# Kernel tuning notes

Hardware: AMD Instinct MI355X
Metric: run time of the kernel (lower is better)

## Reference

```python
import jax, jax.numpy as jnp
import numpy as np


def setup_inputs() -> dict:
    key = jax.random.key(0)
    k1, k2 = jax.random.split(key)
    qs = jax.random.normal(k1, (8, 4096, 1024), dtype=jnp.float32)      # [B, L, D]
    memory = jax.random.normal(k2, (512, 1024), dtype=jnp.float32)       # [M, D]
    return {"qs": qs, "memory": memory}


def reference(qs, memory):
    # s = qs @ memory.T  -> [B, L, M]; permute -> [B, M, L]
    s = jnp.einsum("bld,md->bml", qs, memory)
    # softmax over L (last dim after permute)
    v = jax.nn.softmax(s, axis=2)                 # [B, M, L]
    # r = v @ qs -> [B, M, D]
    r = jnp.einsum("bml,bld->bmd", v, qs)
    return (r, memory)
```

## Files before the change

kernel.cpp:

```cpp
#include <hip/hip_runtime.h>
#include <hip/hip_fp16.h>


#define B_ 8
#define L_ 4096
#define D_ 1024
#define M_ 512

typedef _Float16 halfT;
typedef _Float16 half8 __attribute__((ext_vector_type(8)));
typedef _Float16 half4_t __attribute__((ext_vector_type(4)));
typedef float f32x4 __attribute__((ext_vector_type(4)));

#define OFF_MEM16 0ull
#define SZ_MEM16  (512ull*1024*2)
#define OFF_QS16  (OFF_MEM16 + SZ_MEM16)
#define SZ_QS16   (8ull*4096*1024*2)
#define OFF_S     (OFF_QS16 + SZ_QS16)
#define SZ_S      (8ull*512*4096*4)
#define OFF_P16   (OFF_S + SZ_S)
#define SZ_P16    (8ull*512*4096*2)
#define OFF_INVL  (OFF_P16 + SZ_P16)
#define SZ_INVL   (8ull*512*4)
#define WS_NEED   (OFF_INVL + SZ_INVL)
#define OFF_RP    OFF_S

#define SWZ(n) ((((n)&7) ^ (((n)>>5)&7)))

__device__ __forceinline__ void gload_lds16(const halfT* g, halfT* l) {
  __builtin_amdgcn_global_load_lds(
      (const __attribute__((address_space(1))) unsigned int*)(const void*)g,
      (__attribute__((address_space(3))) unsigned int*)l, 16, 0, 0);
}

__global__ __launch_bounds__(256)
void prep_all(const float* __restrict__ qs, const float* __restrict__ mem,
              halfT* __restrict__ q16, halfT* __restrict__ mem16) {
  int bid = blockIdx.x;
  int tid = threadIdx.x;
  if (bid < 2048) {
    size_t base = (size_t)bid*256 + tid;
    #pragma unroll
    for (int it = 0; it < 8; ++it) {
      size_t i8 = base + (size_t)it*524288;
      size_t row = i8 >> 7;
      int c = (int)(i8 & 127);
      int kt = c >> 3, g = c & 7;
      const float* src = qs + i8*8;
      f32x4 x0 = *(const f32x4*)&src[0];
      f32x4 x1 = *(const f32x4*)&src[4];
      half8 h;
      #pragma unroll
      for (int j = 0; j < 4; ++j) { h[j] = (halfT)x0[j]; h[4+j] = (halfT)x1[j]; }
      *(half8*)&q16[row*1024 + kt*64 + ((g ^ ((int)row & 7)) << 3)] = h;
    }
  } else {
    int i8 = (bid - 2048)*256 + tid;
    int row = i8 >> 7, c = i8 & 127;
    int kt = c >> 3, g = c & 7;
    const float* src = mem + (size_t)i8*8;
    f32x4 x0 = *(const f32x4*)src;
    f32x4 x1 = *(const f32x4*)(src + 4);
    half8 h;
    #pragma unroll
    for (int j = 0; j < 4; ++j) { h[j] = (halfT)x0[j]; h[4+j] = (halfT)x1[j]; }
    *(half8*)&mem16[(size_t)row*1024 + kt*64 + ((g ^ (row & 7)) << 3)] = h;
  }
}

__global__ __launch_bounds__(512, 2)
void gemm_qk(const halfT* __restrict__ mem16, const halfT* __restrict__ qs16,
             float* __restrict__ S)
{
  __shared__ __attribute__((aligned(16))) halfT At[2][256*64];
  __shared__ __attribute__((aligned(16))) halfT Bt[2][256*64];

  int bid = blockIdx.x;
  int swz = (bid & 7)*32 + (bid >> 3);
  int b   = swz >> 5;
  int rem = swz & 31;
  int nt  = rem >> 1;
  int mt  = rem & 1;

  int tid = threadIdx.x;
  int w = tid >> 6, lane = tid & 63, lg = lane >> 4, li = lane & 15;
  int wm = w >> 2, wn = w & 3;
  int sl = li & 7;
  int rA = tid >> 3;
  int cA = (tid & 7)*8;

  const halfT* Ab = mem16 + (size_t)mt*256*1024;
  const halfT* Bb = qs16 + ((size_t)b*L_ + nt*256)*D_;

  f32x4 acc[8][4];
  #pragma unroll
  for (int i=0;i<8;++i)
    #pragma unroll
    for (int j=0;j<4;++j) acc[i][j] = (f32x4){0.f,0.f,0.f,0.f};

#define STAGE_QK(nb_, kt_)                                                     \
  do {                                                                         \
    const halfT* a0 = Ab + (size_t)(kt_)*64 + cA;                              \
    const halfT* b0 = Bb + (size_t)(kt_)*64 + cA;                              \
    _Pragma("unroll")                                                          \
    for (int j = 0; j < 4; ++j) {                                              \
      int r = rA + j*64;                                                       \
      gload_lds16(a0 + (size_t)r*1024, &At[nb_][(tid + j*512)*8]);             \
      gload_lds16(b0 + (size_t)r*1024, &Bt[nb_][(tid + j*512)*8]);             \
    }                                                                          \
  } while (0)

#define COMPUTE_QK(nb_)                                                        \
  do {                                                                         \
    _Pragma("unroll")                                                          \
    for (int ksub = 0; ksub < 2; ++ksub) {                                     \
      int gx = ((ksub*4 + lg) ^ sl) << 3;                                      \
      half8 Af[8], Bf[4];                                                      \
      _Pragma("unroll")                                                        \
      for (int mf = 0; mf < 8; ++mf)                                           \
        Af[mf] = *(const half8*)&At[nb_][(wm*128 + mf*16 + li)*64 + gx];       \
      _Pragma("unroll")                                                        \
      for (int nf = 0; nf < 4; ++nf)                                           \
        Bf[nf] = *(const half8*)&Bt[nb_][(wn*64 + nf*16 + li)*64 + gx];        \
      _Pragma("unroll")                                                        \
      for (int mf = 0; mf < 8; ++mf)                                           \
        _Pragma("unroll")                                                      \
        for (int nf = 0; nf < 4; ++nf)                                         \
          acc[mf][nf] = __builtin_amdgcn_mfma_f32_16x16x32_f16(Af[mf], Bf[nf], acc[mf][nf], 0,0,0); \
    }                                                                          \
  } while (0)

  STAGE_QK(0, 0);
  STAGE_QK(1, 1);
  asm volatile("s_waitcnt vmcnt(8)" ::: "memory");
  __builtin_amdgcn_sched_barrier(0);
  __builtin_amdgcn_s_barrier();

  for (int kt = 0; kt < 16; ++kt) {
    COMPUTE_QK(kt & 1);
    __builtin_amdgcn_s_barrier();
    if (kt + 2 < 16) {
      STAGE_QK(kt & 1, kt + 2);
      asm volatile("s_waitcnt vmcnt(8) lgkmcnt(0)" ::: "memory");
    } else {
      asm volatile("s_waitcnt vmcnt(0) lgkmcnt(0)" ::: "memory");
    }
    __builtin_amdgcn_sched_barrier(0);
    __builtin_amdgcn_s_barrier();
  }
#undef STAGE_QK
#undef COMPUTE_QK

  float* Cb = S + (size_t)b*M_*L_;
  int colbase = nt*256 + wn*64;
  #pragma unroll
  for (int mf = 0; mf < 8; ++mf) {
    #pragma unroll
    for (int r = 0; r < 4; ++r) {
      int row = mt*256 + wm*128 + mf*16 + lg*4 + r;
      #pragma unroll
      for (int nf = 0; nf < 4; ++nf)
        Cb[(size_t)row*L_ + colbase + nf*16 + li] = acc[mf][nf][r];
    }
  }
}

__global__ __launch_bounds__(512, 2)
void gemm_pv(const halfT* __restrict__ P16, const halfT* __restrict__ qs16,
             halfT* __restrict__ rp16)
{
  __shared__ __attribute__((aligned(16))) halfT At[2][256*64];
  __shared__ __attribute__((aligned(16))) halfT Bt[2][256*64];

  int bid = blockIdx.x;
  int swz = (bid & 7)*32 + (bid >> 3);
  int ks  = swz >> 6;
  int rem = swz & 63;
  int b   = rem >> 3;
  int nt  = (rem >> 1) & 3;
  int mt  = rem & 1;

  int tid = threadIdx.x;
  int w = tid >> 6, lane = tid & 63, lg = lane >> 4, li = lane & 15;
  int wm = w >> 2, wn = w & 3;
  int sl = li & 7;

  const halfT* Ab = P16 + (size_t)b*M_*L_ + (size_t)mt*256*L_ + ks*1024;
  const halfT* Bb = qs16 + ((size_t)b*L_ + ks*1024)*D_ + nt*256;
  int krow = tid >> 3;
  int seg  = tid & 7;
  int rs   = krow & 7;

  f32x4 acc[8][4];
  #pragma unroll
  for (int i=0;i<8;++i)
    #pragma unroll
    for (int j=0;j<4;++j) acc[i][j] = (f32x4){0.f,0.f,0.f,0.f};

  half8 hx[4];

#define GLOADB_PV(kt_)                                                         \
  do {                                                                         \
    const halfT* rowp = Bb + (size_t)((kt_)*64 + krow)*D_ + (seg >> 1)*64;     \
    _Pragma("unroll")                                                          \
    for (int j = 0; j < 4; ++j)                                                \
      hx[j] = *(const half8*)(rowp + ((((seg & 1)*4 + j) ^ rs) << 3));         \
  } while (0)

#define STAGEA_PV(nb_, kt_)                                                    \
  do {                                                                         \
    const halfT* a0 = Ab + (size_t)(kt_)*64 + (tid & 7)*8;                     \
    _Pragma("unroll")                                                          \
    for (int j = 0; j < 4; ++j)                                                \
      gload_lds16(a0 + (size_t)((tid >> 3) + j*64)*L_, &At[nb_][(tid + j*512)*8]); \
  } while (0)

#define WRITEB_PV(nb_)                                                         \
  do {                                                                         \
    _Pragma("unroll")                                                          \
    for (int i = 0; i < 32; ++i) {                                             \
      int n_ = seg*32 + i;                                                     \
      Bt[nb_][n_*64 + ((((krow >> 3) ^ SWZ(n_)) << 3)) + (krow & 7)] =         \
          hx[i >> 3][i & 7];                                                   \
    }                                                                          \
  } while (0)

#define COMPUTE_PV(nb_)                                                        \
  do {                                                                         \
    _Pragma("unroll")                                                          \
    for (int ksub = 0; ksub < 2; ++ksub) {                                     \
      int gx = ((ksub*4 + lg) ^ sl) << 3;                                      \
      half8 Af[8], Bf[4];                                                      \
      _Pragma("unroll")                                                        \
      for (int mf = 0; mf < 8; ++mf)                                           \
        Af[mf] = *(const half8*)&At[nb_][(wm*128 + mf*16 + li)*64 + gx];       \
      _Pragma("unroll")                                                        \
      for (int nf = 0; nf < 4; ++nf) {                                         \
        int n_ = wn*64 + nf*16 + li;                                           \
        Bf[nf] = *(const half8*)&Bt[nb_][n_*64 + (((ksub*4 + lg) ^ SWZ(n_)) << 3)]; \
      }                                                                        \
      _Pragma("unroll")                                                        \
      for (int mf = 0; mf < 8; ++mf)                                           \
        _Pragma("unroll")                                                      \
        for (int nf = 0; nf < 4; ++nf)                                         \
          acc[mf][nf] = __builtin_amdgcn_mfma_f32_16x16x32_f16(Af[mf], Bf[nf], acc[mf][nf], 0,0,0); \
    }                                                                          \
  } while (0)

  GLOADB_PV(0);
  STAGEA_PV(0, 0);
  STAGEA_PV(1, 1);
  WRITEB_PV(0);
  GLOADB_PV(1);
  asm volatile("s_waitcnt vmcnt(8) lgkmcnt(0)" ::: "memory");
  __builtin_amdgcn_sched_barrier(0);
  __builtin_amdgcn_s_barrier();

  for (int kt = 0; kt < 16; ++kt) {
    COMPUTE_PV(kt & 1);
    __builtin_amdgcn_s_barrier();
    if (kt + 1 < 16) WRITEB_PV((kt + 1) & 1);
    if (kt + 2 < 16) {
      GLOADB_PV(kt + 2);
      STAGEA_PV(kt & 1, kt + 2);
      asm volatile("s_waitcnt vmcnt(8) lgkmcnt(0)" ::: "memory");
    } else {
      asm volatile("s_waitcnt vmcnt(0) lgkmcnt(0)" ::: "memory");
    }
    __builtin_amdgcn_sched_barrier(0);
    __builtin_amdgcn_s_barrier();
  }
#undef GLOADB_PV
#undef STAGEA_PV
#undef WRITEB_PV
#undef COMPUTE_PV

  halfT* Cb = rp16 + (size_t)ks*((size_t)B_*M_*D_) + (size_t)b*M_*D_;
  int cpbase = nt*256 + wn*64 + li*4;
  #pragma unroll
  for (int mf = 0; mf < 8; ++mf) {
    #pragma unroll
    for (int r = 0; r < 4; ++r) {
      int row = mt*256 + wm*128 + mf*16 + lg*4 + r;
      half4_t hv;
      #pragma unroll
      for (int nf = 0; nf < 4; ++nf) hv[nf] = (halfT)acc[mf][nf][r];
      *(half4_t*)&Cb[(size_t)row*D_ + cpbase] = hv;
    }
  }
}

__global__ __launch_bounds__(256)
void softmax_rows(const float* __restrict__ S, halfT* __restrict__ P,
                  float* __restrict__ invl)
{
  int tid = threadIdx.x;
  int w = tid >> 6, lane = tid & 63;
  int row = blockIdx.x*4 + w;
  int rs  = row & 7;
  const float* src = S + (size_t)row*L_;
  f32x4 v[16];
  float mx = -3.0e38f;
  #pragma unroll
  for (int i = 0; i < 16; ++i) {
    v[i] = *(const f32x4*)&src[(size_t)(i*64 + lane)*4];
    #pragma unroll
    for (int e = 0; e < 4; ++e) mx = fmaxf(mx, v[i][e]);
  }
  #pragma unroll
  for (int off = 1; off < 64; off <<= 1) mx = fmaxf(mx, __shfl_xor(mx, off));

  float sum = 0.f;
  halfT* dst = P + (size_t)row*L_;
  #pragma unroll
  for (int i = 0; i < 16; ++i) {
    half4_t h;
    #pragma unroll
    for (int e = 0; e < 4; ++e) {
      float ev = __expf(v[i][e] - mx);
      sum += ev;
      h[e] = (halfT)ev;
    }
    int c = i*64 + lane;
    int kt = c >> 4, g = (c >> 1) & 7, o = c & 1;
    *(half4_t*)&dst[kt*64 + ((g ^ rs) << 3) + o*4] = h;
  }
  #pragma unroll
  for (int off = 1; off < 64; off <<= 1) sum += __shfl_xor(sum, off);
  if (lane == 0) invl[row] = 1.0f / sum;
}

__global__ __launch_bounds__(256)
void combine_scale(const halfT* __restrict__ rp16, const float* __restrict__ invl,
                   float* __restrict__ out)
{
  int bm = blockIdx.x;
  int t = threadIdx.x;
  size_t off = (size_t)bm*D_ + t*4;
  f32x4 v = (f32x4){0.f,0.f,0.f,0.f};
  #pragma unroll
  for (int s = 0; s < 4; ++s) {
    half4_t h = *(const half4_t*)&rp16[(size_t)s*((size_t)B_*M_*D_) + off];
    #pragma unroll
    for (int j = 0; j < 4; ++j) v[j] += (float)h[j];
  }
  float sc = invl[bm];
  v *= sc;
  int W = (t >> 4) << 6;
  float* ob = out + (size_t)bm*D_;
  #pragma unroll
  for (int j = 0; j < 4; ++j)
    ob[W + j*16 + (t & 15)] = v[j];
}

__global__ void fallback_kernel(const float* __restrict__ qs,
                                const float* __restrict__ mem,
                                float* __restrict__ out)
{
  __shared__ float w_lds[4][4096];
  __shared__ float mem_s[4][1024];
  __shared__ float redb[256];
  int blk = blockIdx.x;
  int b = blk >> 7;
  int m0 = (blk & 127)*4;
  int tid = threadIdx.x;

  for (int i = tid; i < 4*1024; i += 256)
    mem_s[i>>10][i&1023] = mem[(size_t)(m0 + (i>>10))*D_ + (i&1023)];
  __syncthreads();

  float mx[4] = {-3e38f,-3e38f,-3e38f,-3e38f};
  for (int l = tid; l < L_; l += 256) {
    const float* qp = qs + ((size_t)b*L_ + l)*D_;
    float dot[4] = {0,0,0,0};
    for (int dd = 0; dd < D_; dd += 4) {
      f32x4 qv = *(const f32x4*)(qp + dd);
      #pragma unroll
      for (int mi=0; mi<4; ++mi)
        dot[mi] += qv[0]*mem_s[mi][dd] + qv[1]*mem_s[mi][dd+1]
                 + qv[2]*mem_s[mi][dd+2] + qv[3]*mem_s[mi][dd+3];
    }
    #pragma unroll
    for (int mi=0; mi<4; ++mi) { w_lds[mi][l] = dot[mi]; mx[mi] = fmaxf(mx[mi], dot[mi]); }
  }
  float Mv[4], Zv[4];
  for (int mi=0; mi<4; ++mi) {
    redb[tid] = mx[mi]; __syncthreads();
    for (int s=128; s>0; s>>=1) { if (tid<s) redb[tid]=fmaxf(redb[tid],redb[tid+s]); __syncthreads(); }
    Mv[mi] = redb[0]; __syncthreads();
  }
  float sm[4] = {0,0,0,0};
  for (int l = tid; l < L_; l += 256)
    #pragma unroll
    for (int mi=0; mi<4; ++mi) {
      float wv = __expf(w_lds[mi][l] - Mv[mi]);
      w_lds[mi][l] = wv; sm[mi] += wv;
    }
  for (int mi=0; mi<4; ++mi) {
    redb[tid] = sm[mi]; __syncthreads();
    for (int s=128; s>0; s>>=1) { if (tid<s) redb[tid]+=redb[tid+s]; __syncthreads(); }
    Zv[mi] = redb[0]; __syncthreads();
  }
  int d0 = tid*4;
  f32x4 a[4];
  #pragma unroll
  for (int mi=0;mi<4;++mi) a[mi] = (f32x4){0,0,0,0};
  for (int l = 0; l < L_; ++l) {
    f32x4 qv = *(const f32x4*)(qs + ((size_t)b*L_ + l)*D_ + d0);
    #pragma unroll
    for (int mi=0; mi<4; ++mi) a[mi] += qv * w_lds[mi][l];
  }
  #pragma unroll
  for (int mi=0; mi<4; ++mi) {
    float invz = 1.f/Zv[mi];
    #pragma unroll
    for (int c=0; c<4; ++c)
      out[((size_t)b*M_ + m0 + mi)*D_ + d0 + c] = a[mi][c]*invz;
  }
}

extern "C" void kernel_launch(void* const* d_in, const int* in_sizes, int n_in,
                              void* d_out, int out_size, void* d_ws, size_t ws_size,
                              hipStream_t stream) {
  const float* qs  = (const float*)d_in[0];
  const float* mem = (const float*)d_in[1];
  float* out = (float*)d_out;

  hipMemcpyAsync(out + (size_t)B_*M_*D_, mem, (size_t)M_*D_*sizeof(float),
                 hipMemcpyDeviceToDevice, stream);

  if (ws_size >= (size_t)WS_NEED) {
    char* base = (char*)d_ws;
    halfT* mem16 = (halfT*)(base + OFF_MEM16);
    halfT* qs16  = (halfT*)(base + OFF_QS16);
    float* S     = (float*)(base + OFF_S);
    halfT* P16   = (halfT*)(base + OFF_P16);
    float* invl  = (float*)(base + OFF_INVL);
    halfT* rp16  = (halfT*)(base + OFF_RP);

    prep_all<<<2304, 256, 0, stream>>>(qs, mem, qs16, mem16);
    gemm_qk<<<256, 512, 0, stream>>>(mem16, qs16, S);
    softmax_rows<<<1024, 256, 0, stream>>>(S, P16, invl);
    gemm_pv<<<256, 512, 0, stream>>>(P16, qs16, rp16);
    combine_scale<<<4096, 256, 0, stream>>>(rp16, invl, out);
  } else {
    fallback_kernel<<<1024, 256, 0, stream>>>(qs, mem, out);
  }
}
```

Measured before the change: 150.3 us.

## Store fp16 max-shifted scores with per-tile row maxima from QK GEMM

The QK GEMM epilogue now computes a per-row maximum over each 256-column tile, writes it to a small workspace, and stores the scores as fp16 values already shifted by that local max, where it previously wrote fp32 scores. The softmax then reads half as many bytes, combines the 16 tile maxima into a global max, and needs only one pass over the row. The PV GEMM B-row indexing is permuted to match the reordered score column layout. This adds an LDS reduction and extra barrier in the GEMM epilogue, and rounds the shifted scores to fp16, which costs some precision.

```diff
diff --git a/kernel.cpp b/kernel.cpp
--- a/kernel.cpp
+++ b/kernel.cpp
@@ -22,7 +22,9 @@
 #define SZ_P16    (8ull*512*4096*2)
 #define OFF_INVL  (OFF_P16 + SZ_P16)
 #define SZ_INVL   (8ull*512*4)
-#define WS_NEED   (OFF_INVL + SZ_INVL)
+#define OFF_MLOC  (OFF_INVL + SZ_INVL)
+#define SZ_MLOC   (8ull*16*512*4)
+#define WS_NEED   (OFF_MLOC + SZ_MLOC)
 #define OFF_RP    OFF_S
 
 #define SWZ(n) ((((n)&7) ^ (((n)>>5)&7)))
@@ -70,7 +72,7 @@
 
 __global__ __launch_bounds__(512, 2)
 void gemm_qk(const halfT* __restrict__ mem16, const halfT* __restrict__ qs16,
-             float* __restrict__ S)
+             halfT* __restrict__ S16, float* __restrict__ mloc)
 {
   __shared__ __attribute__((aligned(16))) halfT At[2][256*64];
   __shared__ __attribute__((aligned(16))) halfT Bt[2][256*64];
@@ -151,16 +153,47 @@
 #undef STAGE_QK
 #undef COMPUTE_QK
 
-  float* Cb = S + (size_t)b*M_*L_;
-  int colbase = nt*256 + wn*64;
+  float* red = (float*)&At[0][0];
+  float m4[8][4];
+  #pragma unroll
+  for (int mf = 0; mf < 8; ++mf)
+    #pragma unroll
+    for (int r = 0; r < 4; ++r) {
+      float vmax = fmaxf(fmaxf(acc[mf][0][r], acc[mf][1][r]),
+                         fmaxf(acc[mf][2][r], acc[mf][3][r]));
+      #pragma unroll
+      for (int off = 1; off < 16; off <<= 1) vmax = fmaxf(vmax, __shfl_xor(vmax, off));
+      if (li == 0) red[w*128 + mf*16 + lg*4 + r] = vmax;
+    }
+  __syncthreads();
+  #pragma unroll
+  for (int mf = 0; mf < 8; ++mf)
+    #pragma unroll
+    for (int r = 0; r < 4; ++r) {
+      int idx = mf*16 + lg*4 + r;
+      m4[mf][r] = fmaxf(fmaxf(red[(wm*4+0)*128 + idx], red[(wm*4+1)*128 + idx]),
+                        fmaxf(red[(wm*4+2)*128 + idx], red[(wm*4+3)*128 + idx]));
+    }
+  if (wn == 0 && li == 0) {
+    #pragma unroll
+    for (int mf = 0; mf < 8; ++mf)
+      #pragma unroll
+      for (int r = 0; r < 4; ++r) {
+        int m = mt*256 + wm*128 + mf*16 + lg*4 + r;
+        mloc[((size_t)b*16 + nt)*M_ + m] = m4[mf][r];
+      }
+  }
+  halfT* Cb = S16 + (size_t)b*M_*L_;
+  int cpb = nt*256 + wn*64 + li*4;
   #pragma unroll
   for (int mf = 0; mf < 8; ++mf) {
     #pragma unroll
     for (int r = 0; r < 4; ++r) {
       int row = mt*256 + wm*128 + mf*16 + lg*4 + r;
-      #pragma unroll
-      for (int nf = 0; nf < 4; ++nf)
-        Cb[(size_t)row*L_ + colbase + nf*16 + li] = acc[mf][nf][r];
+      half4_t hv;
+      #pragma unroll
+      for (int nf = 0; nf < 4; ++nf) hv[nf] = (halfT)(acc[mf][nf][r] - m4[mf][r]);
+      *(half4_t*)&Cb[(size_t)row*L_ + cpb] = hv;
     }
   }
 }
@@ -189,7 +222,8 @@
   const halfT* Bb = qs16 + ((size_t)b*L_ + ks*1024)*D_ + nt*256;
   int krow = tid >> 3;
   int seg  = tid & 7;
-  int rs   = krow & 7;
+  int pinv = ((krow & 3) << 4) | (krow >> 2);
+  int rs   = pinv & 7;
 
   f32x4 acc[8][4];
   #pragma unroll
@@ -201,7 +235,7 @@
 
 #define GLOADB_PV(kt_)                                                         \
   do {                                                                         \
-    const halfT* rowp = Bb + (size_t)((kt_)*64 + krow)*D_ + (seg >> 1)*64;     \
+    const halfT* rowp = Bb + (size_t)((kt_)*64 + pinv)*D_ + (seg >> 1)*64;     \
     _Pragma("unroll")                                                          \
     for (int j = 0; j < 4; ++j)                                                \
       hx[j] = *(const half8*)(rowp + ((((seg & 1)*4 + j) ^ rs) << 3));         \
@@ -291,33 +325,30 @@
 }
 
 __global__ __launch_bounds__(256)
-void softmax_rows(const float* __restrict__ S, halfT* __restrict__ P,
-                  float* __restrict__ invl)
+void softmax_rows(const halfT* __restrict__ S16, const float* __restrict__ mloc,
+                  halfT* __restrict__ P, float* __restrict__ invl)
 {
   int tid = threadIdx.x;
   int w = tid >> 6, lane = tid & 63;
   int row = blockIdx.x*4 + w;
+  int b = row >> 9, m = row & 511;
   int rs  = row & 7;
-  const float* src = S + (size_t)row*L_;
-  f32x4 v[16];
-  float mx = -3.0e38f;
+  float mv = (lane < 16) ? mloc[((size_t)b*16 + lane)*M_ + m] : -3.0e38f;
+  float M = mv;
+  #pragma unroll
+  for (int off = 1; off < 64; off <<= 1) M = fmaxf(M, __shfl_xor(M, off));
+
+  const halfT* src = S16 + (size_t)row*L_;
+  halfT* dst = P + (size_t)row*L_;
+  float sum = 0.f;
   #pragma unroll
   for (int i = 0; i < 16; ++i) {
-    v[i] = *(const f32x4*)&src[(size_t)(i*64 + lane)*4];
-    #pragma unroll
-    for (int e = 0; e < 4; ++e) mx = fmaxf(mx, v[i][e]);
-  }
-  #pragma unroll
-  for (int off = 1; off < 64; off <<= 1) mx = fmaxf(mx, __shfl_xor(mx, off));
-
-  float sum = 0.f;
-  halfT* dst = P + (size_t)row*L_;
-  #pragma unroll
-  for (int i = 0; i < 16; ++i) {
+    float di = __shfl(mv, i) - M;
+    half4_t s4 = *(const half4_t*)&src[(size_t)(i*64 + lane)*4];
     half4_t h;
     #pragma unroll
     for (int e = 0; e < 4; ++e) {
-      float ev = __expf(v[i][e] - mx);
+      float ev = __expf((float)s4[e] + di);
       sum += ev;
       h[e] = (halfT)ev;
     }
@@ -433,14 +464,15 @@
     char* base = (char*)d_ws;
     halfT* mem16 = (halfT*)(base + OFF_MEM16);
     halfT* qs16  = (halfT*)(base + OFF_QS16);
-    float* S     = (float*)(base + OFF_S);
+    halfT* S16   = (halfT*)(base + OFF_S);
     halfT* P16   = (halfT*)(base + OFF_P16);
     float* invl  = (float*)(base + OFF_INVL);
+    float* mloc  = (float*)(base + OFF_MLOC);
     halfT* rp16  = (halfT*)(base + OFF_RP);
 
     prep_all<<<2304, 256, 0, stream>>>(qs, mem, qs16, mem16);
-    gemm_qk<<<256, 512, 0, stream>>>(mem16, qs16, S);
-    softmax_rows<<<1024, 256, 0, stream>>>(S, P16, invl);
+    gemm_qk<<<256, 512, 0, stream>>>(mem16, qs16, S16, mloc);
+    softmax_rows<<<1024, 256, 0, stream>>>(S16, mloc, P16, invl);
     gemm_pv<<<256, 512, 0, stream>>>(P16, qs16, rp16);
     combine_scale<<<4096, 256, 0, stream>>>(rp16, invl, out);
   } else {
```

Measured after the change: 144.9 us, median of 2. 3.6% less time.
